# Optimization experiments

Measured on AMD Instinct MI355X. Metric: run time of the kernel, lower is better.

## Reference

```python
import jax, jax.numpy as jnp
import numpy as np

B, C, H, W = 4, 256, 64, 64
C8 = C // 8  # q/k projection dim = 32

def setup_inputs() -> dict:
    key = jax.random.key(0)
    ks = jax.random.split(key, 6)
    s = 0.02
    return {
        "x": jax.random.normal(ks[0], (B, C, H, W), dtype=jnp.float32),
        "wq": jax.random.normal(ks[1], (C8, C), dtype=jnp.float32) * s,
        "bq": jnp.zeros((C8,), dtype=jnp.float32),
        "wk": jax.random.normal(ks[2], (C8, C), dtype=jnp.float32) * s,
        "bk": jnp.zeros((C8,), dtype=jnp.float32),
        "wv": jax.random.normal(ks[3], (C, C), dtype=jnp.float32) * s,
        "bv": jnp.zeros((C,), dtype=jnp.float32),
        "wo": jax.random.normal(ks[4], (C, C), dtype=jnp.float32) * s,
        "bo": jnp.zeros((C,), dtype=jnp.float32),
        "scale": jnp.zeros((1,), dtype=jnp.float32),
    }

def reference(x, wq, bq, wk, bk, wv, bv, wo, bo, scale):
    b, c, h, w = x.shape
    n = h * w
    xf = x.reshape(b, c, n)  # (B, C, N)
    # 1x1 convs are channel-mixing GEMMs
    q = jnp.einsum('oc,bcn->bon', wq, xf) + bq[None, :, None]  # (B, C8, N)
    k = jnp.einsum('oc,bcn->bon', wk, xf) + bk[None, :, None]  # (B, C8, N)
    v = jnp.einsum('oc,bcn->bon', wv, xf) + bv[None, :, None]  # (B, C,  N)
    inv_sqrt = 1.0 / jnp.sqrt(jnp.asarray(c // 8, dtype=x.dtype))
    scores = jnp.einsum('bon,bom->bnm', q, k) * inv_sqrt  # (B, N, N): query n, key m
    attn = jax.nn.softmax(scores, axis=-1)
    # torch: bmm(value, attn^T) -> attended[:, :, n] = sum_m v[:, :, m] * attn[n, m]
    attended = jnp.einsum('bcm,bnm->bcn', v, attn)  # (B, C, N)
    out = jnp.einsum('oc,bcn->bon', wo, attended) + bo[None, :, None]
    out = out.reshape(b, c, h, w)
    return x + scale[0] * out
```

## Files before the change

### kernel.cpp

```cpp
#include <hip/hip_runtime.h>
#include <stdint.h>

#define B_ 4
#define C_ 256
#define C8_ 32
#define N_ 4096
#define LOG2E 1.4426950408889634f
#define INV_SQRT32 0.17677669529663689f

typedef __bf16 bf16x8 __attribute__((ext_vector_type(8)));
typedef float f32x16 __attribute__((ext_vector_type(16)));
typedef unsigned int uint4v __attribute__((ext_vector_type(4)));

__device__ __forceinline__ uint16_t f2bf(float f) {
  uint32_t u = __builtin_bit_cast(uint32_t, f);
  return (uint16_t)((u + 0x7FFFu + ((u >> 16) & 1u)) >> 16);
}
__device__ __forceinline__ uint32_t pack2bf(float a, float b) {
  uint32_t ua = __builtin_bit_cast(uint32_t, a);
  uint32_t ub = __builtin_bit_cast(uint32_t, b);
  ua = (ua + 0x7FFFu + ((ua >> 16) & 1u)) >> 16;
  ub = (ub + 0x7FFFu + ((ub >> 16) & 1u)) & 0xFFFF0000u;
  return ua | ub;
}
__device__ __forceinline__ bf16x8 load_bf8(const uint16_t* p) {
  uint4v u = *(const uint4v*)p;
  return __builtin_bit_cast(bf16x8, u);
}
__device__ __forceinline__ f32x16 mfma32(bf16x8 a, bf16x8 b, f32x16 c) {
  return __builtin_amdgcn_mfma_f32_32x32x16_bf16(a, b, c, 0, 0, 0);
}
__device__ __forceinline__ f32x16 mfma32_f8(long a, long b, f32x16 c) {
  return __builtin_amdgcn_mfma_f32_32x32x16_fp8_fp8(a, b, c, 0, 0, 0);
}

__global__ void k_transpose_cast(const float* __restrict__ x,
                                 uint16_t* __restrict__ xb2) {
  __shared__ uint16_t st[32][64];
  int b = blockIdx.z, c0 = blockIdx.y * 32, n0 = blockIdx.x * 64;
  int tid = threadIdx.x;
  {
    int r = tid >> 4;
    int l = (tid & 15) * 4;
    const float* xp = x + ((size_t)b * C_ + c0) * N_ + n0;
    float4 v0 = *(const float4*)(xp + (size_t)r * N_ + l);
    float4 v1 = *(const float4*)(xp + (size_t)(r + 16) * N_ + l);
    st[r][l + 0] = f2bf(v0.x); st[r][l + 1] = f2bf(v0.y);
    st[r][l + 2] = f2bf(v0.z); st[r][l + 3] = f2bf(v0.w);
    st[r + 16][l + 0] = f2bf(v1.x); st[r + 16][l + 1] = f2bf(v1.y);
    st[r + 16][l + 2] = f2bf(v1.z); st[r + 16][l + 3] = f2bf(v1.w);
  }
  __syncthreads();
  int cg = tid >> 6, n = tid & 63;
  uint4v o;
#pragma unroll
  for (int p = 0; p < 4; p++) {
    o[p] = (uint32_t)st[cg * 8 + 2 * p][n] | ((uint32_t)st[cg * 8 + 2 * p + 1][n] << 16);
  }
  *(uint4v*)(xb2 + ((size_t)(b * 32 + (c0 >> 3) + cg) * N_ + n0 + n) * 8) = o;
}

__global__ void k_cast_weights(const float* __restrict__ wq, const float* __restrict__ wk,
                               const float* __restrict__ wv, const float* __restrict__ wo,
                               uint16_t* __restrict__ wqb, uint16_t* __restrict__ wkb,
                               uint16_t* __restrict__ wvb, uint16_t* __restrict__ wob) {
  int i = blockIdx.x * 256 + threadIdx.x;
  if (i < 8192) {
    int o = i >> 8, c = i & 255;
    wqb[((size_t)(c >> 3) * 32 + o) * 8 + (c & 7)] = f2bf(wq[i]);
  } else if (i < 16384) {
    int j = i - 8192; int o = j >> 8, c = j & 255;
    wkb[((size_t)(c >> 3) * 32 + o) * 8 + (c & 7)] = f2bf(wk[j]);
  } else if (i < 81920) {
    int j = i - 16384; int o = j >> 8, c = j & 255;
    wvb[((size_t)(c >> 3) * 256 + o) * 8 + (c & 7)] = f2bf(wv[j]);
  } else {
    int j = i - 81920; int o = j >> 8, c = j & 255;
    wob[((size_t)(c >> 3) * 256 + o) * 8 + (c & 7)] = f2bf(wo[j]);
  }
}

__global__ void k_proj_qk(const uint16_t* __restrict__ xb2,
                          const uint16_t* __restrict__ wqb, const float* __restrict__ bq,
                          const uint16_t* __restrict__ wkb, const float* __restrict__ bk,
                          uint16_t* __restrict__ Qb, uint16_t* __restrict__ Kt) {
  int b = blockIdx.z;
  int which = blockIdx.y;
  int n0 = blockIdx.x * 32;
  int lane = threadIdx.x;
  int h = lane >> 5, ln = lane & 31;
  const uint16_t* W = which ? wkb : wqb;
  const float* bias = which ? bk : bq;
  float sc = which ? 1.0f : INV_SQRT32;

  f32x16 acc;
#pragma unroll
  for (int i = 0; i < 16; i++) acc[i] = 0.0f;
  const uint16_t* xbase = xb2 + (size_t)(b * 32) * N_ * 8 + (size_t)(n0 + ln) * 8;
#pragma unroll 4
  for (int c = 0; c < C_; c += 16) {
    bf16x8 a = load_bf8(W + ((size_t)(c / 8 + h) * 32 + ln) * 8);
    bf16x8 bb = load_bf8(xbase + (size_t)(c / 8 + h) * N_ * 8);
    acc = mfma32(a, bb, acc);
  }
#pragma unroll
  for (int g = 0; g < 4; g++) {
    int row = g * 8 + h * 4;
    uint32_t p0 = pack2bf((acc[4 * g + 0] + bias[row + 0]) * sc,
                          (acc[4 * g + 1] + bias[row + 1]) * sc);
    uint32_t p1 = pack2bf((acc[4 * g + 2] + bias[row + 2]) * sc,
                          (acc[4 * g + 3] + bias[row + 3]) * sc);
    uint2 pr; pr.x = p0; pr.y = p1;
    if (which == 0) {
      *(uint2*)(Qb + ((size_t)b * N_ + n0 + ln) * C8_ + row) = pr;
    } else {
      *(uint2*)(Kt + ((size_t)(b * 4 + g) * N_ + n0 + ln) * 8 + h * 4) = pr;
    }
  }
}

__global__ void k_proj_v(const uint16_t* __restrict__ xb2,
                         const uint16_t* __restrict__ wvb, const float* __restrict__ bv,
                         uint8_t* __restrict__ V8) {
  int b = blockIdx.z;
  int n0 = blockIdx.x * 32;
  int wave = threadIdx.x >> 6;
  int o0 = blockIdx.y * 128 + wave * 32;
  int lane = threadIdx.x & 63;
  int h = lane >> 5, ln = lane & 31;
  f32x16 acc;
#pragma unroll
  for (int i = 0; i < 16; i++) acc[i] = 0.0f;
  const uint16_t* xbase = xb2 + (size_t)(b * 32) * N_ * 8 + (size_t)(n0 + ln) * 8;
#pragma unroll 4
  for (int c = 0; c < C_; c += 16) {
    bf16x8 a = load_bf8(wvb + ((size_t)(c / 8 + h) * 256 + o0 + ln) * 8);
    bf16x8 bb = load_bf8(xbase + (size_t)(c / 8 + h) * N_ * 8);
    acc = mfma32(a, bb, acc);
  }
  int kg = b * 512 + (n0 >> 3) + (ln >> 3);
  int j = ln & 7;
#pragma unroll
  for (int r = 0; r < 16; r++) {
    int row = (r & 3) + 8 * (r >> 2) + 4 * h;
    int o = o0 + row;
    float v = acc[r] + bv[o];
    int pk = __builtin_amdgcn_cvt_pk_fp8_f32(v, v, 0, false);
    V8[((size_t)kg * 256 + o) * 8 + j] = (uint8_t)(pk & 0xff);
  }
}

__global__ __launch_bounds__(512, 4) void k_attn(
    const uint16_t* __restrict__ Qb, const uint16_t* __restrict__ Kt,
    const uint8_t* __restrict__ V8, uint16_t* __restrict__ A_kb) {
  __shared__ uint32_t sO[8][4][8][64];
  __shared__ float smax[8][32];
  __shared__ float sl[4][32];

  int b = blockIdx.x;
  int qt = blockIdx.y;
  int wave = threadIdx.x >> 6;
  int kw = wave >> 1, cw = wave & 1;
  int lane = threadIdx.x & 63;
  int h = lane >> 5, ln = lane & 31;
  int qi = qt * 32 + ln;

  const uint16_t* qrow = Qb + ((size_t)b * N_ + qi) * C8_;
  bf16x8 qf1 = load_bf8(qrow + h * 8);
  bf16x8 qf2 = load_bf8(qrow + 16 + h * 8);
  const uint16_t* k1base = Kt + ((size_t)(b * 4 + h) * N_) * 8;
  const uint16_t* k2base = Kt + ((size_t)(b * 4 + 2 + h) * N_) * 8;

  float pmax = -1e30f;
  for (int m0 = wave * 512; m0 < wave * 512 + 512; m0 += 32) {
    bf16x8 ka1 = load_bf8(k1base + (size_t)(m0 + ln) * 8);
    bf16x8 ka2 = load_bf8(k2base + (size_t)(m0 + ln) * 8);
    f32x16 S;
#pragma unroll
    for (int i = 0; i < 16; i++) S[i] = 0.0f;
    S = mfma32(ka1, qf1, S);
    S = mfma32(ka2, qf2, S);
#pragma unroll
    for (int r = 0; r < 16; r++) pmax = fmaxf(pmax, S[r]);
  }
  pmax = fmaxf(pmax, __shfl_xor(pmax, 32, 64));
  if (h == 0) smax[wave][ln] = pmax;
  __syncthreads();
  float mg = smax[0][ln];
#pragma unroll
  for (int p = 1; p < 8; p++) mg = fmaxf(mg, smax[p][ln]);
  float mgl = mg * LOG2E;

  f32x16 O[4];
#pragma unroll
  for (int t = 0; t < 4; t++)
#pragma unroll
    for (int r = 0; r < 16; r++) O[t][r] = 0.0f;
  float lsum = 0.0f;
  const uint8_t* vb = V8 + (size_t)(b * 512) * 256 * 8;

  for (int m0 = kw * 1024; m0 < kw * 1024 + 1024; m0 += 32) {
    bf16x8 ka1 = load_bf8(k1base + (size_t)(m0 + ln) * 8);
    bf16x8 ka2 = load_bf8(k2base + (size_t)(m0 + ln) * 8);
    f32x16 S;
#pragma unroll
    for (int i = 0; i < 16; i++) S[i] = 0.0f;
    S = mfma32(ka1, qf1, S);
    S = mfma32(ka2, qf2, S);

    float P[16];
#pragma unroll
    for (int r = 0; r < 16; r++) {
      P[r] = __builtin_amdgcn_exp2f(S[r] * LOG2E - mgl);
      lsum += P[r];
    }
    uint32_t w0 = __builtin_amdgcn_cvt_pk_fp8_f32(P[0], P[1], 0, false);
    w0 = __builtin_amdgcn_cvt_pk_fp8_f32(P[2], P[3], w0, true);
    uint32_t w1 = __builtin_amdgcn_cvt_pk_fp8_f32(P[4], P[5], 0, false);
    w1 = __builtin_amdgcn_cvt_pk_fp8_f32(P[6], P[7], w1, true);
    uint32_t w2 = __builtin_amdgcn_cvt_pk_fp8_f32(P[8], P[9], 0, false);
    w2 = __builtin_amdgcn_cvt_pk_fp8_f32(P[10], P[11], w2, true);
    uint32_t w3 = __builtin_amdgcn_cvt_pk_fp8_f32(P[12], P[13], 0, false);
    w3 = __builtin_amdgcn_cvt_pk_fp8_f32(P[14], P[15], w3, true);
    uint32_t s0 = h ? w0 : w1;
    uint32_t s1 = h ? w2 : w3;
    uint32_t r0 = (uint32_t)__shfl_xor((int)s0, 32, 64);
    uint32_t r1 = (uint32_t)__shfl_xor((int)s1, 32, 64);
    uint32_t a0lo = h ? r0 : w0, a0hi = h ? w1 : r0;
    uint32_t a1lo = h ? r1 : w2, a1hi = h ? w3 : r1;
    long pa = (long)(((uint64_t)a0hi << 32) | a0lo);
    long pb = (long)(((uint64_t)a1hi << 32) | a1lo);

    const uint8_t* v1 = vb + ((size_t)((m0 >> 3) + h) * 256 + cw * 128 + ln) * 8;
#pragma unroll
    for (int t = 0; t < 4; t++) {
      uint2 u1 = *(const uint2*)(v1 + t * 256);
      uint2 u2 = *(const uint2*)(v1 + 4096 + t * 256);
      long va = (long)(((uint64_t)u1.y << 32) | u1.x);
      long vc = (long)(((uint64_t)u2.y << 32) | u2.x);
      O[t] = mfma32_f8(va, pa, O[t]);
      O[t] = mfma32_f8(vc, pb, O[t]);
    }
  }

  lsum += __shfl_xor(lsum, 32, 64);
  if (cw == 0 && h == 0) sl[kw][ln] = lsum;
#pragma unroll
  for (int t = 0; t < 4; t++)
#pragma unroll
    for (int i = 0; i < 8; i++)
      sO[wave][t][i][lane] = pack2bf(O[t][2 * i], O[t][2 * i + 1]);
  __syncthreads();

  float lg = sl[0][ln] + sl[1][ln] + sl[2][ln] + sl[3][ln];
  float inv = 1.0f / lg;

  int cw_s = wave >> 2, lt = wave & 3;
  float acc[16];
#pragma unroll
  for (int r = 0; r < 16; r++) acc[r] = 0.0f;
#pragma unroll
  for (int k = 0; k < 4; k++) {
    int src = k * 2 + cw_s;
#pragma unroll
    for (int i = 0; i < 8; i++) {
      uint32_t u = sO[src][lt][i][lane];
      acc[2 * i]     += __builtin_bit_cast(float, u << 16);
      acc[2 * i + 1] += __builtin_bit_cast(float, u & 0xFFFF0000u);
    }
  }
#pragma unroll
  for (int g = 0; g < 4; g++) {
    uint2 pr;
    pr.x = pack2bf(acc[4 * g + 0] * inv, acc[4 * g + 1] * inv);
    pr.y = pack2bf(acc[4 * g + 2] * inv, acc[4 * g + 3] * inv);
    *(uint2*)(A_kb + ((size_t)(b * 32 + wave * 4 + g) * N_ + qi) * 8 + h * 4) = pr;
  }
}

__global__ void k_out(const uint16_t* __restrict__ A_kb,
                      const uint16_t* __restrict__ wob, const float* __restrict__ bo,
                      const float* __restrict__ x, const float* __restrict__ scale,
                      float* __restrict__ out) {
  int b = blockIdx.z;
  int n0 = blockIdx.x * 32;
  int wave = threadIdx.x >> 6;
  int o0 = blockIdx.y * 128 + wave * 32;
  int lane = threadIdx.x & 63;
  int h = lane >> 5, ln = lane & 31;
  f32x16 acc;
#pragma unroll
  for (int i = 0; i < 16; i++) acc[i] = 0.0f;
  const uint16_t* abase = A_kb + (size_t)(b * 32) * N_ * 8 + (size_t)(n0 + ln) * 8;
#pragma unroll 4
  for (int c = 0; c < C_; c += 16) {
    bf16x8 a = load_bf8(wob + ((size_t)(c / 8 + h) * 256 + o0 + ln) * 8);
    bf16x8 bb = load_bf8(abase + (size_t)(c / 8 + h) * N_ * 8);
    acc = mfma32(a, bb, acc);
  }
  float s = scale[0];
#pragma unroll
  for (int r = 0; r < 16; r++) {
    int row = (r & 3) + 8 * (r >> 2) + 4 * h;
    int o = o0 + row;
    size_t idx = ((size_t)b * C_ + o) * N_ + n0 + ln;
    out[idx] = x[idx] + s * (acc[r] + bo[o]);
  }
}

extern "C" void kernel_launch(void* const* d_in, const int* in_sizes, int n_in,
                              void* d_out, int out_size, void* d_ws, size_t ws_size,
                              hipStream_t stream) {
  const float* x  = (const float*)d_in[0];
  const float* wq = (const float*)d_in[1];
  const float* bq = (const float*)d_in[2];
  const float* wk = (const float*)d_in[3];
  const float* bk = (const float*)d_in[4];
  const float* wv = (const float*)d_in[5];
  const float* bv = (const float*)d_in[6];
  const float* wo = (const float*)d_in[7];
  const float* bo = (const float*)d_in[8];
  const float* scale = (const float*)d_in[9];
  float* out = (float*)d_out;

  char* w = (char*)d_ws;
  uint16_t* xb2  = (uint16_t*)(w);
  uint16_t* Qb   = (uint16_t*)(w + (8u << 20));
  uint16_t* Kt   = (uint16_t*)(w + (9u << 20));
  uint8_t*  V8   = (uint8_t*)(w + (10u << 20));
  uint16_t* A_kb = (uint16_t*)(w + (18u << 20));
  uint16_t* Wqb  = (uint16_t*)(w + (26u << 20));
  uint16_t* Wkb = Wqb + 32 * 256;
  uint16_t* Wvb = Wkb + 32 * 256;
  uint16_t* Wob = Wvb + 256 * 256;

  k_transpose_cast<<<dim3(N_ / 64, C_ / 32, B_), 256, 0, stream>>>(x, xb2);
  k_cast_weights<<<576, 256, 0, stream>>>(wq, wk, wv, wo, Wqb, Wkb, Wvb, Wob);
  k_proj_qk<<<dim3(N_ / 32, 2, B_), 64, 0, stream>>>(xb2, Wqb, bq, Wkb, bk, Qb, Kt);
  k_proj_v<<<dim3(N_ / 32, 2, B_), 256, 0, stream>>>(xb2, Wvb, bv, V8);
  k_attn<<<dim3(B_, N_ / 32), 512, 0, stream>>>(Qb, Kt, V8, A_kb);
  k_out<<<dim3(N_ / 32, 2, B_), 256, 0, stream>>>(A_kb, Wob, bo, x, scale, out);
}
```

Measured before the change: 166.0 us.

## Process two query tiles per attention block and fuse QKV projection kernels

The attention kernel now handles 64 queries per block (two 32-query tiles), so each K and V load is reused across two sets of MFMAs. The grid is halved and launch bounds relaxed to two blocks per CU. The separate Q/K and V projection kernels merge into one kernel that computes 64 columns per block, and the output projection kernel also processes 64 columns per block to reuse weight loads. This trades more registers (two sets of O accumulators) and fewer blocks for less global memory traffic and fewer launches.

```diff
diff --git a/kernel.cpp b/kernel.cpp
--- a/kernel.cpp
+++ b/kernel.cpp
@@ -32,6 +32,25 @@
 }
 __device__ __forceinline__ f32x16 mfma32_f8(long a, long b, f32x16 c) {
   return __builtin_amdgcn_mfma_f32_32x32x16_fp8_fp8(a, b, c, 0, 0, 0);
+}
+
+__device__ __forceinline__ void pack_p_fp8(const float* P, int h, long& pa, long& pb) {
+  uint32_t w0 = __builtin_amdgcn_cvt_pk_fp8_f32(P[0], P[1], 0, false);
+  w0 = __builtin_amdgcn_cvt_pk_fp8_f32(P[2], P[3], w0, true);
+  uint32_t w1 = __builtin_amdgcn_cvt_pk_fp8_f32(P[4], P[5], 0, false);
+  w1 = __builtin_amdgcn_cvt_pk_fp8_f32(P[6], P[7], w1, true);
+  uint32_t w2 = __builtin_amdgcn_cvt_pk_fp8_f32(P[8], P[9], 0, false);
+  w2 = __builtin_amdgcn_cvt_pk_fp8_f32(P[10], P[11], w2, true);
+  uint32_t w3 = __builtin_amdgcn_cvt_pk_fp8_f32(P[12], P[13], 0, false);
+  w3 = __builtin_amdgcn_cvt_pk_fp8_f32(P[14], P[15], w3, true);
+  uint32_t s0 = h ? w0 : w1;
+  uint32_t s1 = h ? w2 : w3;
+  uint32_t r0 = (uint32_t)__shfl_xor((int)s0, 32, 64);
+  uint32_t r1 = (uint32_t)__shfl_xor((int)s1, 32, 64);
+  uint32_t a0lo = h ? r0 : w0, a0hi = h ? w1 : r0;
+  uint32_t a1lo = h ? r1 : w2, a1hi = h ? w3 : r1;
+  pa = (long)(((uint64_t)a0hi << 32) | a0lo);
+  pb = (long)(((uint64_t)a1hi << 32) | a1lo);
 }
 
 __global__ void k_transpose_cast(const float* __restrict__ x,
@@ -80,201 +99,221 @@
   }
 }
 
-__global__ void k_proj_qk(const uint16_t* __restrict__ xb2,
-                          const uint16_t* __restrict__ wqb, const float* __restrict__ bq,
-                          const uint16_t* __restrict__ wkb, const float* __restrict__ bk,
-                          uint16_t* __restrict__ Qb, uint16_t* __restrict__ Kt) {
-  int b = blockIdx.z;
-  int which = blockIdx.y;
-  int n0 = blockIdx.x * 32;
-  int lane = threadIdx.x;
-  int h = lane >> 5, ln = lane & 31;
-  const uint16_t* W = which ? wkb : wqb;
-  const float* bias = which ? bk : bq;
-  float sc = which ? 1.0f : INV_SQRT32;
-
-  f32x16 acc;
-#pragma unroll
-  for (int i = 0; i < 16; i++) acc[i] = 0.0f;
-  const uint16_t* xbase = xb2 + (size_t)(b * 32) * N_ * 8 + (size_t)(n0 + ln) * 8;
-#pragma unroll 4
-  for (int c = 0; c < C_; c += 16) {
-    bf16x8 a = load_bf8(W + ((size_t)(c / 8 + h) * 32 + ln) * 8);
-    bf16x8 bb = load_bf8(xbase + (size_t)(c / 8 + h) * N_ * 8);
-    acc = mfma32(a, bb, acc);
-  }
-#pragma unroll
-  for (int g = 0; g < 4; g++) {
-    int row = g * 8 + h * 4;
-    uint32_t p0 = pack2bf((acc[4 * g + 0] + bias[row + 0]) * sc,
-                          (acc[4 * g + 1] + bias[row + 1]) * sc);
-    uint32_t p1 = pack2bf((acc[4 * g + 2] + bias[row + 2]) * sc,
-                          (acc[4 * g + 3] + bias[row + 3]) * sc);
-    uint2 pr; pr.x = p0; pr.y = p1;
-    if (which == 0) {
-      *(uint2*)(Qb + ((size_t)b * N_ + n0 + ln) * C8_ + row) = pr;
-    } else {
-      *(uint2*)(Kt + ((size_t)(b * 4 + g) * N_ + n0 + ln) * 8 + h * 4) = pr;
-    }
-  }
-}
-
-__global__ void k_proj_v(const uint16_t* __restrict__ xb2,
-                         const uint16_t* __restrict__ wvb, const float* __restrict__ bv,
-                         uint8_t* __restrict__ V8) {
-  int b = blockIdx.z;
-  int n0 = blockIdx.x * 32;
+__global__ __launch_bounds__(320) void k_proj_qkv(
+    const uint16_t* __restrict__ xb2,
+    const uint16_t* __restrict__ wqb, const float* __restrict__ bq,
+    const uint16_t* __restrict__ wkb, const float* __restrict__ bk,
+    const uint16_t* __restrict__ wvb, const float* __restrict__ bv,
+    uint16_t* __restrict__ Qb, uint16_t* __restrict__ Kt, uint8_t* __restrict__ V8) {
+  int b = blockIdx.y;
+  int n0 = blockIdx.x * 64;
   int wave = threadIdx.x >> 6;
-  int o0 = blockIdx.y * 128 + wave * 32;
   int lane = threadIdx.x & 63;
   int h = lane >> 5, ln = lane & 31;
-  f32x16 acc;
-#pragma unroll
-  for (int i = 0; i < 16; i++) acc[i] = 0.0f;
-  const uint16_t* xbase = xb2 + (size_t)(b * 32) * N_ * 8 + (size_t)(n0 + ln) * 8;
+
+  if (wave == 0) {
+#pragma unroll
+    for (int s = 0; s < 2; s++) {
+      int nb = n0 + s * 32;
+      const uint16_t* xbase = xb2 + (size_t)(b * 32) * N_ * 8 + (size_t)(nb + ln) * 8;
+      f32x16 aq, ak;
+#pragma unroll
+      for (int i = 0; i < 16; i++) { aq[i] = 0.0f; ak[i] = 0.0f; }
 #pragma unroll 4
-  for (int c = 0; c < C_; c += 16) {
-    bf16x8 a = load_bf8(wvb + ((size_t)(c / 8 + h) * 256 + o0 + ln) * 8);
-    bf16x8 bb = load_bf8(xbase + (size_t)(c / 8 + h) * N_ * 8);
-    acc = mfma32(a, bb, acc);
-  }
-  int kg = b * 512 + (n0 >> 3) + (ln >> 3);
-  int j = ln & 7;
-#pragma unroll
-  for (int r = 0; r < 16; r++) {
-    int row = (r & 3) + 8 * (r >> 2) + 4 * h;
-    int o = o0 + row;
-    float v = acc[r] + bv[o];
-    int pk = __builtin_amdgcn_cvt_pk_fp8_f32(v, v, 0, false);
-    V8[((size_t)kg * 256 + o) * 8 + j] = (uint8_t)(pk & 0xff);
-  }
-}
-
-__global__ __launch_bounds__(512, 4) void k_attn(
+      for (int c = 0; c < C_; c += 16) {
+        bf16x8 bb = load_bf8(xbase + (size_t)(c / 8 + h) * N_ * 8);
+        aq = mfma32(load_bf8(wqb + ((size_t)(c / 8 + h) * 32 + ln) * 8), bb, aq);
+        ak = mfma32(load_bf8(wkb + ((size_t)(c / 8 + h) * 32 + ln) * 8), bb, ak);
+      }
+#pragma unroll
+      for (int g = 0; g < 4; g++) {
+        int row = g * 8 + h * 4;
+        uint2 pq, pk;
+        pq.x = pack2bf((aq[4 * g + 0] + bq[row + 0]) * INV_SQRT32,
+                       (aq[4 * g + 1] + bq[row + 1]) * INV_SQRT32);
+        pq.y = pack2bf((aq[4 * g + 2] + bq[row + 2]) * INV_SQRT32,
+                       (aq[4 * g + 3] + bq[row + 3]) * INV_SQRT32);
+        *(uint2*)(Qb + ((size_t)b * N_ + nb + ln) * C8_ + row) = pq;
+        pk.x = pack2bf(ak[4 * g + 0] + bk[row + 0], ak[4 * g + 1] + bk[row + 1]);
+        pk.y = pack2bf(ak[4 * g + 2] + bk[row + 2], ak[4 * g + 3] + bk[row + 3]);
+        *(uint2*)(Kt + ((size_t)(b * 4 + g) * N_ + nb + ln) * 8 + h * 4) = pk;
+      }
+    }
+  } else {
+    int o0 = (wave - 1) * 64;
+#pragma unroll
+    for (int s = 0; s < 2; s++) {
+      int nb = n0 + s * 32;
+      const uint16_t* xbase = xb2 + (size_t)(b * 32) * N_ * 8 + (size_t)(nb + ln) * 8;
+      f32x16 a0, a1;
+#pragma unroll
+      for (int i = 0; i < 16; i++) { a0[i] = 0.0f; a1[i] = 0.0f; }
+#pragma unroll 4
+      for (int c = 0; c < C_; c += 16) {
+        bf16x8 bb = load_bf8(xbase + (size_t)(c / 8 + h) * N_ * 8);
+        a0 = mfma32(load_bf8(wvb + ((size_t)(c / 8 + h) * 256 + o0 + ln) * 8), bb, a0);
+        a1 = mfma32(load_bf8(wvb + ((size_t)(c / 8 + h) * 256 + o0 + 32 + ln) * 8), bb, a1);
+      }
+      int kg = b * 512 + (nb >> 3) + (ln >> 3);
+      int j = ln & 7;
+#pragma unroll
+      for (int r = 0; r < 16; r++) {
+        int row = (r & 3) + 8 * (r >> 2) + 4 * h;
+        float v0 = a0[r] + bv[o0 + row];
+        float v1 = a1[r] + bv[o0 + 32 + row];
+        int p0 = __builtin_amdgcn_cvt_pk_fp8_f32(v0, v0, 0, false);
+        int p1 = __builtin_amdgcn_cvt_pk_fp8_f32(v1, v1, 0, false);
+        V8[((size_t)kg * 256 + o0 + row) * 8 + j] = (uint8_t)(p0 & 0xff);
+        V8[((size_t)kg * 256 + o0 + 32 + row) * 8 + j] = (uint8_t)(p1 & 0xff);
+      }
+    }
+  }
+}
+
+__global__ __launch_bounds__(512, 2) void k_attn(
     const uint16_t* __restrict__ Qb, const uint16_t* __restrict__ Kt,
     const uint8_t* __restrict__ V8, uint16_t* __restrict__ A_kb) {
   __shared__ uint32_t sO[8][4][8][64];
-  __shared__ float smax[8][32];
+  __shared__ float smax[8][2][32];
   __shared__ float sl[4][32];
 
-  int b = blockIdx.x;
-  int qt = blockIdx.y;
+  int bx = blockIdx.x;
+  int b = bx >> 1;
+  int q0 = (blockIdx.y + 32 * (bx & 1)) * 64;
   int wave = threadIdx.x >> 6;
   int kw = wave >> 1, cw = wave & 1;
   int lane = threadIdx.x & 63;
   int h = lane >> 5, ln = lane & 31;
-  int qi = qt * 32 + ln;
-
-  const uint16_t* qrow = Qb + ((size_t)b * N_ + qi) * C8_;
-  bf16x8 qf1 = load_bf8(qrow + h * 8);
-  bf16x8 qf2 = load_bf8(qrow + 16 + h * 8);
+
+  bf16x8 qf[2][2];
+#pragma unroll
+  for (int qt = 0; qt < 2; qt++) {
+    const uint16_t* qrow = Qb + ((size_t)b * N_ + q0 + qt * 32 + ln) * C8_;
+    qf[qt][0] = load_bf8(qrow + h * 8);
+    qf[qt][1] = load_bf8(qrow + 16 + h * 8);
+  }
   const uint16_t* k1base = Kt + ((size_t)(b * 4 + h) * N_) * 8;
   const uint16_t* k2base = Kt + ((size_t)(b * 4 + 2 + h) * N_) * 8;
 
-  float pmax = -1e30f;
+  float pmax0 = -1e30f, pmax1 = -1e30f;
   for (int m0 = wave * 512; m0 < wave * 512 + 512; m0 += 32) {
     bf16x8 ka1 = load_bf8(k1base + (size_t)(m0 + ln) * 8);
     bf16x8 ka2 = load_bf8(k2base + (size_t)(m0 + ln) * 8);
-    f32x16 S;
-#pragma unroll
-    for (int i = 0; i < 16; i++) S[i] = 0.0f;
-    S = mfma32(ka1, qf1, S);
-    S = mfma32(ka2, qf2, S);
-#pragma unroll
-    for (int r = 0; r < 16; r++) pmax = fmaxf(pmax, S[r]);
-  }
-  pmax = fmaxf(pmax, __shfl_xor(pmax, 32, 64));
-  if (h == 0) smax[wave][ln] = pmax;
+    f32x16 S0, S1;
+#pragma unroll
+    for (int i = 0; i < 16; i++) { S0[i] = 0.0f; S1[i] = 0.0f; }
+    S0 = mfma32(ka1, qf[0][0], S0); S0 = mfma32(ka2, qf[0][1], S0);
+    S1 = mfma32(ka1, qf[1][0], S1); S1 = mfma32(ka2, qf[1][1], S1);
+#pragma unroll
+    for (int r = 0; r < 16; r++) {
+      pmax0 = fmaxf(pmax0, S0[r]);
+      pmax1 = fmaxf(pmax1, S1[r]);
+    }
+  }
+  pmax0 = fmaxf(pmax0, __shfl_xor(pmax0, 32, 64));
+  pmax1 = fmaxf(pmax1, __shfl_xor(pmax1, 32, 64));
+  if (h == 0) { smax[wave][0][ln] = pmax0; smax[wave][1][ln] = pmax1; }
   __syncthreads();
-  float mg = smax[0][ln];
-#pragma unroll
-  for (int p = 1; p < 8; p++) mg = fmaxf(mg, smax[p][ln]);
-  float mgl = mg * LOG2E;
-
-  f32x16 O[4];
+  float mg0 = smax[0][0][ln], mg1 = smax[0][1][ln];
+#pragma unroll
+  for (int p = 1; p < 8; p++) {
+    mg0 = fmaxf(mg0, smax[p][0][ln]);
+    mg1 = fmaxf(mg1, smax[p][1][ln]);
+  }
+  float mgl0 = mg0 * LOG2E, mgl1 = mg1 * LOG2E;
+
+  f32x16 O0[4], O1[4];
 #pragma unroll
   for (int t = 0; t < 4; t++)
 #pragma unroll
-    for (int r = 0; r < 16; r++) O[t][r] = 0.0f;
-  float lsum = 0.0f;
-  const uint8_t* vb = V8 + (size_t)(b * 512) * 256 * 8;
+    for (int r = 0; r < 16; r++) { O0[t][r] = 0.0f; O1[t][r] = 0.0f; }
+  float ls0 = 0.0f, ls1 = 0.0f;
+  const uint8_t* vbase = V8 + (size_t)(b * 512) * 2048 + cw * 1024 + ln * 8;
 
   for (int m0 = kw * 1024; m0 < kw * 1024 + 1024; m0 += 32) {
     bf16x8 ka1 = load_bf8(k1base + (size_t)(m0 + ln) * 8);
     bf16x8 ka2 = load_bf8(k2base + (size_t)(m0 + ln) * 8);
-    f32x16 S;
-#pragma unroll
-    for (int i = 0; i < 16; i++) S[i] = 0.0f;
-    S = mfma32(ka1, qf1, S);
-    S = mfma32(ka2, qf2, S);
-
-    float P[16];
-#pragma unroll
-    for (int r = 0; r < 16; r++) {
-      P[r] = __builtin_amdgcn_exp2f(S[r] * LOG2E - mgl);
-      lsum += P[r];
-    }
-    uint32_t w0 = __builtin_amdgcn_cvt_pk_fp8_f32(P[0], P[1], 0, false);
-    w0 = __builtin_amdgcn_cvt_pk_fp8_f32(P[2], P[3], w0, true);
-    uint32_t w1 = __builtin_amdgcn_cvt_pk_fp8_f32(P[4], P[5], 0, false);
-    w1 = __builtin_amdgcn_cvt_pk_fp8_f32(P[6], P[7], w1, true);
-    uint32_t w2 = __builtin_amdgcn_cvt_pk_fp8_f32(P[8], P[9], 0, false);
-    w2 = __builtin_amdgcn_cvt_pk_fp8_f32(P[10], P[11], w2, true);
-    uint32_t w3 = __builtin_amdgcn_cvt_pk_fp8_f32(P[12], P[13], 0, false);
-    w3 = __builtin_amdgcn_cvt_pk_fp8_f32(P[14], P[15], w3, true);
-    uint32_t s0 = h ? w0 : w1;
-    uint32_t s1 = h ? w2 : w3;
-    uint32_t r0 = (uint32_t)__shfl_xor((int)s0, 32, 64);
-    uint32_t r1 = (uint32_t)__shfl_xor((int)s1, 32, 64);
-    uint32_t a0lo = h ? r0 : w0, a0hi = h ? w1 : r0;
-    uint32_t a1lo = h ? r1 : w2, a1hi = h ? w3 : r1;
-    long pa = (long)(((uint64_t)a0hi << 32) | a0lo);
-    long pb = (long)(((uint64_t)a1hi << 32) | a1lo);
-
-    const uint8_t* v1 = vb + ((size_t)((m0 >> 3) + h) * 256 + cw * 128 + ln) * 8;
+    long pa0, pb0, pa1, pb1;
+    {
+      f32x16 S;
+#pragma unroll
+      for (int i = 0; i < 16; i++) S[i] = 0.0f;
+      S = mfma32(ka1, qf[0][0], S); S = mfma32(ka2, qf[0][1], S);
+      float P[16];
+#pragma unroll
+      for (int r = 0; r < 16; r++) {
+        P[r] = __builtin_amdgcn_exp2f(S[r] * LOG2E - mgl0);
+        ls0 += P[r];
+      }
+      pack_p_fp8(P, h, pa0, pb0);
+    }
+    {
+      f32x16 S;
+#pragma unroll
+      for (int i = 0; i < 16; i++) S[i] = 0.0f;
+      S = mfma32(ka1, qf[1][0], S); S = mfma32(ka2, qf[1][1], S);
+      float P[16];
+#pragma unroll
+      for (int r = 0; r < 16; r++) {
+        P[r] = __builtin_amdgcn_exp2f(S[r] * LOG2E - mgl1);
+        ls1 += P[r];
+      }
+      pack_p_fp8(P, h, pa1, pb1);
+    }
+    const uint8_t* vp = vbase + (size_t)((m0 >> 3) + h) * 2048;
 #pragma unroll
     for (int t = 0; t < 4; t++) {
-      uint2 u1 = *(const uint2*)(v1 + t * 256);
-      uint2 u2 = *(const uint2*)(v1 + 4096 + t * 256);
+      uint2 u1 = *(const uint2*)(vp + t * 256);
+      uint2 u2 = *(const uint2*)(vp + 4096 + t * 256);
       long va = (long)(((uint64_t)u1.y << 32) | u1.x);
       long vc = (long)(((uint64_t)u2.y << 32) | u2.x);
-      O[t] = mfma32_f8(va, pa, O[t]);
-      O[t] = mfma32_f8(vc, pb, O[t]);
-    }
-  }
-
-  lsum += __shfl_xor(lsum, 32, 64);
-  if (cw == 0 && h == 0) sl[kw][ln] = lsum;
-#pragma unroll
-  for (int t = 0; t < 4; t++)
-#pragma unroll
-    for (int i = 0; i < 8; i++)
-      sO[wave][t][i][lane] = pack2bf(O[t][2 * i], O[t][2 * i + 1]);
-  __syncthreads();
-
-  float lg = sl[0][ln] + sl[1][ln] + sl[2][ln] + sl[3][ln];
-  float inv = 1.0f / lg;
-
-  int cw_s = wave >> 2, lt = wave & 3;
-  float acc[16];
-#pragma unroll
-  for (int r = 0; r < 16; r++) acc[r] = 0.0f;
-#pragma unroll
-  for (int k = 0; k < 4; k++) {
-    int src = k * 2 + cw_s;
-#pragma unroll
-    for (int i = 0; i < 8; i++) {
-      uint32_t u = sO[src][lt][i][lane];
-      acc[2 * i]     += __builtin_bit_cast(float, u << 16);
-      acc[2 * i + 1] += __builtin_bit_cast(float, u & 0xFFFF0000u);
-    }
-  }
-#pragma unroll
-  for (int g = 0; g < 4; g++) {
-    uint2 pr;
-    pr.x = pack2bf(acc[4 * g + 0] * inv, acc[4 * g + 1] * inv);
-    pr.y = pack2bf(acc[4 * g + 2] * inv, acc[4 * g + 3] * inv);
-    *(uint2*)(A_kb + ((size_t)(b * 32 + wave * 4 + g) * N_ + qi) * 8 + h * 4) = pr;
+      O0[t] = mfma32_f8(va, pa0, O0[t]);
+      O0[t] = mfma32_f8(vc, pb0, O0[t]);
+      O1[t] = mfma32_f8(va, pa1, O1[t]);
+      O1[t] = mfma32_f8(vc, pb1, O1[t]);
+    }
+  }
+  ls0 += __shfl_xor(ls0, 32, 64);
+  ls1 += __shfl_xor(ls1, 32, 64);
+
+#pragma unroll
+  for (int qt = 0; qt < 2; qt++) {
+    __syncthreads();
+#pragma unroll
+    for (int t = 0; t < 4; t++)
+#pragma unroll
+      for (int i = 0; i < 8; i++) {
+        float lo = qt ? O1[t][2 * i] : O0[t][2 * i];
+        float hi = qt ? O1[t][2 * i + 1] : O0[t][2 * i + 1];
+        sO[wave][t][i][lane] = pack2bf(lo, hi);
+      }
+    if (cw == 0 && h == 0) sl[kw][ln] = qt ? ls1 : ls0;
+    __syncthreads();
+
+    float lg = sl[0][ln] + sl[1][ln] + sl[2][ln] + sl[3][ln];
+    float inv = 1.0f / lg;
+    int c = wave;
+    int cs = c >> 2, lt = c & 3;
+    float acc[16];
+#pragma unroll
+    for (int r = 0; r < 16; r++) acc[r] = 0.0f;
+#pragma unroll
+    for (int k = 0; k < 4; k++) {
+      int src = k * 2 + cs;
+#pragma unroll
+      for (int i = 0; i < 8; i++) {
+        uint32_t u = sO[src][lt][i][lane];
+        acc[2 * i]     += __builtin_bit_cast(float, u << 16);
+        acc[2 * i + 1] += __builtin_bit_cast(float, u & 0xFFFF0000u);
+      }
+    }
+#pragma unroll
+    for (int g = 0; g < 4; g++) {
+      uint2 pr;
+      pr.x = pack2bf(acc[4 * g + 0] * inv, acc[4 * g + 1] * inv);
+      pr.y = pack2bf(acc[4 * g + 2] * inv, acc[4 * g + 3] * inv);
+      *(uint2*)(A_kb + ((size_t)(b * 32 + c * 4 + g) * N_ + q0 + qt * 32 + ln) * 8 + h * 4) = pr;
+    }
   }
 }
 
@@ -283,28 +322,30 @@
                       const float* __restrict__ x, const float* __restrict__ scale,
                       float* __restrict__ out) {
   int b = blockIdx.z;
-  int n0 = blockIdx.x * 32;
+  int n0 = blockIdx.x * 64;
   int wave = threadIdx.x >> 6;
   int o0 = blockIdx.y * 128 + wave * 32;
   int lane = threadIdx.x & 63;
   int h = lane >> 5, ln = lane & 31;
-  f32x16 acc;
-#pragma unroll
-  for (int i = 0; i < 16; i++) acc[i] = 0.0f;
-  const uint16_t* abase = A_kb + (size_t)(b * 32) * N_ * 8 + (size_t)(n0 + ln) * 8;
+  f32x16 acc0, acc1;
+#pragma unroll
+  for (int i = 0; i < 16; i++) { acc0[i] = 0.0f; acc1[i] = 0.0f; }
+  const uint16_t* ab0 = A_kb + (size_t)(b * 32) * N_ * 8 + (size_t)(n0 + ln) * 8;
+  const uint16_t* ab1 = ab0 + 32 * 8;
 #pragma unroll 4
   for (int c = 0; c < C_; c += 16) {
     bf16x8 a = load_bf8(wob + ((size_t)(c / 8 + h) * 256 + o0 + ln) * 8);
-    bf16x8 bb = load_bf8(abase + (size_t)(c / 8 + h) * N_ * 8);
-    acc = mfma32(a, bb, acc);
+    acc0 = mfma32(a, load_bf8(ab0 + (size_t)(c / 8 + h) * N_ * 8), acc0);
+    acc1 = mfma32(a, load_bf8(ab1 + (size_t)(c / 8 + h) * N_ * 8), acc1);
   }
   float s = scale[0];
 #pragma unroll
   for (int r = 0; r < 16; r++) {
     int row = (r & 3) + 8 * (r >> 2) + 4 * h;
     int o = o0 + row;
-    size_t idx = ((size_t)b * C_ + o) * N_ + n0 + ln;
-    out[idx] = x[idx] + s * (acc[r] + bo[o]);
+    size_t idx0 = ((size_t)b * C_ + o) * N_ + n0 + ln;
+    out[idx0] = x[idx0] + s * (acc0[r] + bo[o]);
+    out[idx0 + 32] = x[idx0 + 32] + s * (acc1[r] + bo[o]);
   }
 }
 
@@ -336,8 +377,8 @@
 
   k_transpose_cast<<<dim3(N_ / 64, C_ / 32, B_), 256, 0, stream>>>(x, xb2);
   k_cast_weights<<<576, 256, 0, stream>>>(wq, wk, wv, wo, Wqb, Wkb, Wvb, Wob);
-  k_proj_qk<<<dim3(N_ / 32, 2, B_), 64, 0, stream>>>(xb2, Wqb, bq, Wkb, bk, Qb, Kt);
-  k_proj_v<<<dim3(N_ / 32, 2, B_), 256, 0, stream>>>(xb2, Wvb, bv, V8);
-  k_attn<<<dim3(B_, N_ / 32), 512, 0, stream>>>(Qb, Kt, V8, A_kb);
-  k_out<<<dim3(N_ / 32, 2, B_), 256, 0, stream>>>(A_kb, Wob, bo, x, scale, out);
-}
+  k_proj_qkv<<<dim3(N_ / 64, B_), 320, 0, stream>>>(xb2, Wqb, bq, Wkb, bk, Wvb, bv,
+                                                    Qb, Kt, V8);
+  k_attn<<<dim3(8, 32), 512, 0, stream>>>(Qb, Kt, V8, A_kb);
+  k_out<<<dim3(N_ / 64, 2, B_), 256, 0, stream>>>(A_kb, Wob, bo, x, scale, out);
+}
```

Result: no change. 163.1 us (-1.8%).
